# Kernel optimization log

Hardware: AMD Instinct MI355X
Metric: run time of the kernel (lower is better)

Reference implementation:

```python
import jax, jax.numpy as jnp
import numpy as np

S, B, D = 2048, 32, 1024
H = 16
DIM = D // H  # 64 per-head dim
EPS = 1e-5


def setup_inputs() -> dict:
    key = jax.random.key(0)
    k1, k2, k3 = jax.random.split(key, 3)
    src = jax.random.normal(k1, (S, B, D), dtype=jnp.float32)
    # per-head bracket Linear(2*dim -> dim), stacked over heads
    bound = 1.0 / np.sqrt(2 * DIM)
    W = jax.random.uniform(k2, (H, 2 * DIM, DIM), minval=-bound, maxval=bound, dtype=jnp.float32)
    b = jax.random.uniform(k3, (H, DIM), minval=-bound, maxval=bound, dtype=jnp.float32)
    # shared LayerNorm(d_model) params (default init: gamma=1, beta=0)
    gamma = jnp.ones((D,), dtype=jnp.float32)
    beta = jnp.zeros((D,), dtype=jnp.float32)
    return {"src": src, "W": W, "b": b, "gamma": gamma, "beta": beta}


def reference(src, W, b, gamma, beta):
    def layer_norm(x):
        mu = jnp.mean(x, axis=-1, keepdims=True)
        var = jnp.mean(jnp.square(x - mu), axis=-1, keepdims=True)
        return (x - mu) * jax.lax.rsqrt(var + EPS) * gamma + beta

    def step(c, x):
        # c, x: [B, D]; mode='base': y_h = GELU(Linear_h([c_h; x_h])), new context = x
        ch = c.reshape(B, H, DIM)
        xh = x.reshape(B, H, DIM)
        cat = jnp.concatenate([ch, xh], axis=-1)              # [B, H, 2*DIM]
        y = jax.nn.gelu(jnp.einsum('bhk,hkd->bhd', cat, W) + b, approximate=False)
        c_new = layer_norm(x)                                  # LN(context)=LN(x)
        y_out = layer_norm(y.reshape(B, D))
        return c_new, y_out

    c0 = jnp.zeros((B, D), dtype=src.dtype)
    _, ys = jax.lax.scan(step, c0, src)
    return ys  # [S, B, D]
```

## Files before the change

### kernel.cpp

```cpp
#include <hip/hip_runtime.h>

#define SS 2048
#define BB 32
#define DD 1024
#define HH 16

typedef unsigned short u16;
typedef unsigned int u32;
using f32x4 = __attribute__((ext_vector_type(4))) float;
using bf16x8 = __attribute__((ext_vector_type(8))) short;

__device__ __forceinline__ u16 f2bf(float x) {
  union { float f; u32 u; } c; c.f = x;
  u32 r = c.u + 0x7fffu + ((c.u >> 16) & 1u);
  return (u16)(r >> 16);
}
__device__ __forceinline__ float bf2f(u32 h) {
  union { u32 u; float f; } c; c.u = h << 16; return c.f;
}
__device__ __forceinline__ int swzb(int row, int col) {
  return ((row << 11) + (col << 1)) ^ ((row & 7) << 4);
}
__device__ __forceinline__ void st_lds8(u16* base, int row, int col, const u16* v) {
  uint4 pk;
  pk.x = (u32)v[0] | ((u32)v[1] << 16);
  pk.y = (u32)v[2] | ((u32)v[3] << 16);
  pk.z = (u32)v[4] | ((u32)v[5] << 16);
  pk.w = (u32)v[6] | ((u32)v[7] << 16);
  *reinterpret_cast<uint4*>(reinterpret_cast<char*>(base) + swzb(row, col)) = pk;
}
__device__ __forceinline__ uint4 ld_lds8(const u16* base, int row, int col) {
  return *reinterpret_cast<const uint4*>(reinterpret_cast<const char*>(base) + swzb(row, col));
}
__device__ __forceinline__ bf16x8 ld_afrag(const u16* base, int row, int col) {
  return *reinterpret_cast<const bf16x8*>(reinterpret_cast<const char*>(base) + swzb(row, col));
}
__device__ __forceinline__ void st_lds1(u16* base, int row, int col, u16 v) {
  *reinterpret_cast<u16*>(reinterpret_cast<char*>(base) + swzb(row, col)) = v;
}

__global__ void prep_w(const float* __restrict__ W, u16* __restrict__ Wf) {
  const int o = blockIdx.x * 256 + threadIdx.x;
  const int l = o & 63;
  const int tile = o >> 6;
  const int nt = tile & 3, ks = (tile >> 2) & 3, h = tile >> 4;
  const int d = nt * 16 + (l & 15);
  const int kb = ks * 32 + 8 * (l >> 4);
  u16 v[8];
#pragma unroll
  for (int j = 0; j < 8; ++j) v[j] = f2bf(W[(h * 128 + kb + j) * 64 + d]);
  uint4 pk;
  pk.x = (u32)v[0] | ((u32)v[1] << 16);
  pk.y = (u32)v[2] | ((u32)v[3] << 16);
  pk.z = (u32)v[4] | ((u32)v[5] << 16);
  pk.w = (u32)v[6] | ((u32)v[7] << 16);
  reinterpret_cast<uint4*>(Wf)[o] = pk;
}

__global__ __launch_bounds__(1024) void lienet_main(
    const float* __restrict__ src, const u16* __restrict__ Wf,
    const float* __restrict__ bias, const float* __restrict__ gamma,
    const float* __restrict__ beta, float* __restrict__ out) {
  __shared__ __align__(16) u16 cbuf[BB * DD];
  __shared__ __align__(16) u16 xbuf[BB * DD];

  const int bid = blockIdx.x;
  const int t = (bid & 7) * 256 + (bid >> 3);

  const int tid = threadIdx.x;
  const int wave = tid >> 6;
  const int lane = tid & 63;
  const int colbase = lane * 16;

#pragma unroll
  for (int rr = 0; rr < 2; ++rr) {
    const int row = wave * 2 + rr;
    {
      const float4* p = reinterpret_cast<const float4*>(src + ((size_t)t * BB + row) * DD + colbase);
      u16 v[16];
#pragma unroll
      for (int q = 0; q < 4; ++q) {
        float4 f = p[q];
        v[q * 4 + 0] = f2bf(f.x); v[q * 4 + 1] = f2bf(f.y);
        v[q * 4 + 2] = f2bf(f.z); v[q * 4 + 3] = f2bf(f.w);
      }
      st_lds8(xbuf, row, colbase, v);
      st_lds8(xbuf, row, colbase + 8, v + 8);
    }
    if (t == 0) {
      u16 v[16];
#pragma unroll
      for (int j = 0; j < 16; ++j) v[j] = 0;
      st_lds8(cbuf, row, colbase, v);
      st_lds8(cbuf, row, colbase + 8, v + 8);
    } else {
      const float4* p = reinterpret_cast<const float4*>(src + ((size_t)(t - 1) * BB + row) * DD + colbase);
      float f[16];
      float s1 = 0.f, s2 = 0.f;
#pragma unroll
      for (int q = 0; q < 4; ++q) {
        float4 fv = p[q];
        f[q * 4 + 0] = fv.x; f[q * 4 + 1] = fv.y;
        f[q * 4 + 2] = fv.z; f[q * 4 + 3] = fv.w;
      }
#pragma unroll
      for (int j = 0; j < 16; ++j) { s1 += f[j]; s2 += f[j] * f[j]; }
#pragma unroll
      for (int off = 32; off; off >>= 1) { s1 += __shfl_xor(s1, off); s2 += __shfl_xor(s2, off); }
      const float mu = s1 * (1.f / 1024.f);
      const float rs = rsqrtf(s2 * (1.f / 1024.f) - mu * mu + 1e-5f);
      const float4* gp = reinterpret_cast<const float4*>(gamma + colbase);
      const float4* bp = reinterpret_cast<const float4*>(beta + colbase);
      u16 v[16];
#pragma unroll
      for (int q = 0; q < 4; ++q) {
        float4 gv = gp[q], bv = bp[q];
        v[q * 4 + 0] = f2bf((f[q * 4 + 0] - mu) * rs * gv.x + bv.x);
        v[q * 4 + 1] = f2bf((f[q * 4 + 1] - mu) * rs * gv.y + bv.y);
        v[q * 4 + 2] = f2bf((f[q * 4 + 2] - mu) * rs * gv.z + bv.z);
        v[q * 4 + 3] = f2bf((f[q * 4 + 3] - mu) * rs * gv.w + bv.w);
      }
      st_lds8(cbuf, row, colbase, v);
      st_lds8(cbuf, row, colbase + 8, v + 8);
    }
  }
  __syncthreads();

  const int h = wave;
  f32x4 acc[2][4];
#pragma unroll
  for (int mt = 0; mt < 2; ++mt)
#pragma unroll
    for (int nt = 0; nt < 4; ++nt) acc[mt][nt] = (f32x4){0.f, 0.f, 0.f, 0.f};

  const int arow = lane & 15;
  const int kb = 8 * (lane >> 4);
#pragma unroll
  for (int ks = 0; ks < 4; ++ks) {
    const u16* sb = (ks < 2) ? cbuf : xbuf;
    const int col = h * 64 + (ks & 1) * 32 + kb;
    bf16x8 a0 = ld_afrag(sb, arow, col);
    bf16x8 a1 = ld_afrag(sb, arow + 16, col);
    const uint4* wp = reinterpret_cast<const uint4*>(Wf) + ((h * 4 + ks) * 4) * 64 + lane;
#pragma unroll
    for (int nt = 0; nt < 4; ++nt) {
      uint4 wv = wp[nt * 64];
      bf16x8 bfr = *reinterpret_cast<bf16x8*>(&wv);
      acc[0][nt] = __builtin_amdgcn_mfma_f32_16x16x32_bf16(a0, bfr, acc[0][nt], 0, 0, 0);
      acc[1][nt] = __builtin_amdgcn_mfma_f32_16x16x32_bf16(a1, bfr, acc[1][nt], 0, 0, 0);
    }
  }

#pragma unroll
  for (int nt = 0; nt < 4; ++nt) {
    const int dcol = h * 64 + nt * 16 + (lane & 15);
    const float bv = bias[dcol];
#pragma unroll
    for (int mt = 0; mt < 2; ++mt) {
#pragma unroll
      for (int r = 0; r < 4; ++r) {
        const int row = mt * 16 + (lane >> 4) * 4 + r;
        const float v = acc[mt][nt][r] + bv;
        const float gel = 0.5f * v * (1.0f + erff(v * 0.70710678118654752f));
        st_lds1(cbuf, row, dcol, f2bf(gel));
      }
    }
  }
  __syncthreads();

#pragma unroll
  for (int rr = 0; rr < 2; ++rr) {
    const int row = wave * 2 + rr;
    uint4 g0 = ld_lds8(cbuf, row, colbase);
    uint4 g1 = ld_lds8(cbuf, row, colbase + 8);
    float vals[16];
    vals[0] = bf2f(g0.x & 0xffffu); vals[1] = bf2f(g0.x >> 16);
    vals[2] = bf2f(g0.y & 0xffffu); vals[3] = bf2f(g0.y >> 16);
    vals[4] = bf2f(g0.z & 0xffffu); vals[5] = bf2f(g0.z >> 16);
    vals[6] = bf2f(g0.w & 0xffffu); vals[7] = bf2f(g0.w >> 16);
    vals[8] = bf2f(g1.x & 0xffffu); vals[9] = bf2f(g1.x >> 16);
    vals[10] = bf2f(g1.y & 0xffffu); vals[11] = bf2f(g1.y >> 16);
    vals[12] = bf2f(g1.z & 0xffffu); vals[13] = bf2f(g1.z >> 16);
    vals[14] = bf2f(g1.w & 0xffffu); vals[15] = bf2f(g1.w >> 16);
    float s1 = 0.f, s2 = 0.f;
#pragma unroll
    for (int j = 0; j < 16; ++j) { s1 += vals[j]; s2 += vals[j] * vals[j]; }
#pragma unroll
    for (int off = 32; off; off >>= 1) { s1 += __shfl_xor(s1, off); s2 += __shfl_xor(s2, off); }
    const float mu = s1 * (1.f / 1024.f);
    const float rs = rsqrtf(s2 * (1.f / 1024.f) - mu * mu + 1e-5f);
    const float4* gp = reinterpret_cast<const float4*>(gamma + colbase);
    const float4* bp = reinterpret_cast<const float4*>(beta + colbase);
    float* op = out + ((size_t)t * BB + row) * DD + colbase;
#pragma unroll
    for (int q = 0; q < 4; ++q) {
      float4 gv = gp[q], bv = bp[q];
      float4 o;
      o.x = (vals[q * 4 + 0] - mu) * rs * gv.x + bv.x;
      o.y = (vals[q * 4 + 1] - mu) * rs * gv.y + bv.y;
      o.z = (vals[q * 4 + 2] - mu) * rs * gv.z + bv.z;
      o.w = (vals[q * 4 + 3] - mu) * rs * gv.w + bv.w;
      reinterpret_cast<float4*>(op)[q] = o;
    }
  }
}

extern "C" void kernel_launch(void* const* d_in, const int* in_sizes, int n_in,
                              void* d_out, int out_size, void* d_ws, size_t ws_size,
                              hipStream_t stream) {
  const float* src = (const float*)d_in[0];
  const float* W = (const float*)d_in[1];
  const float* bias = (const float*)d_in[2];
  const float* gamma = (const float*)d_in[3];
  const float* beta = (const float*)d_in[4];
  float* out = (float*)d_out;
  u16* Wf = (u16*)d_ws;

  prep_w<<<64, 256, 0, stream>>>(W, Wf);
  lienet_main<<<SS, 1024, 0, stream>>>(src, Wf, bias, gamma, beta, out);
}
```

Before: 258.5 us.

## Split each timestep into 8-row blocks and fuse output LayerNorm in registers

New measurement: 228.4 us. -11.6%, faster.

```diff
diff --git a/kernel.cpp b/kernel.cpp
--- a/kernel.cpp
+++ b/kernel.cpp
@@ -4,6 +4,7 @@
 #define BB 32
 #define DD 1024
 #define HH 16
+#define RB 8
 
 typedef unsigned short u16;
 typedef unsigned int u32;
@@ -15,28 +16,30 @@
   u32 r = c.u + 0x7fffu + ((c.u >> 16) & 1u);
   return (u16)(r >> 16);
 }
-__device__ __forceinline__ float bf2f(u32 h) {
-  union { u32 u; float f; } c; c.u = h << 16; return c.f;
-}
 __device__ __forceinline__ int swzb(int row, int col) {
   return ((row << 11) + (col << 1)) ^ ((row & 7) << 4);
 }
-__device__ __forceinline__ void st_lds8(u16* base, int row, int col, const u16* v) {
+__device__ __forceinline__ void st_lds8(u16* base, int row, int col,
+                                        float4 a, float4 b) {
   uint4 pk;
-  pk.x = (u32)v[0] | ((u32)v[1] << 16);
-  pk.y = (u32)v[2] | ((u32)v[3] << 16);
-  pk.z = (u32)v[4] | ((u32)v[5] << 16);
-  pk.w = (u32)v[6] | ((u32)v[7] << 16);
+  pk.x = (u32)f2bf(a.x) | ((u32)f2bf(a.y) << 16);
+  pk.y = (u32)f2bf(a.z) | ((u32)f2bf(a.w) << 16);
+  pk.z = (u32)f2bf(b.x) | ((u32)f2bf(b.y) << 16);
+  pk.w = (u32)f2bf(b.z) | ((u32)f2bf(b.w) << 16);
   *reinterpret_cast<uint4*>(reinterpret_cast<char*>(base) + swzb(row, col)) = pk;
 }
-__device__ __forceinline__ uint4 ld_lds8(const u16* base, int row, int col) {
-  return *reinterpret_cast<const uint4*>(reinterpret_cast<const char*>(base) + swzb(row, col));
+__device__ __forceinline__ void st_lds8z(u16* base, int row, int col) {
+  uint4 pk; pk.x = pk.y = pk.z = pk.w = 0u;
+  *reinterpret_cast<uint4*>(reinterpret_cast<char*>(base) + swzb(row, col)) = pk;
 }
 __device__ __forceinline__ bf16x8 ld_afrag(const u16* base, int row, int col) {
   return *reinterpret_cast<const bf16x8*>(reinterpret_cast<const char*>(base) + swzb(row, col));
 }
-__device__ __forceinline__ void st_lds1(u16* base, int row, int col, u16 v) {
-  *reinterpret_cast<u16*>(reinterpret_cast<char*>(base) + swzb(row, col)) = v;
+__device__ __forceinline__ float gelu_f(float v) {
+  const float u2 = 1.5957691216057308f * v * __builtin_fmaf(0.044715f, v * v, 1.0f);
+  const float e = __expf(u2);
+  const float th = 1.0f - 2.0f * __builtin_amdgcn_rcpf(e + 1.0f);
+  return 0.5f * v * (1.0f + th);
 }
 
 __global__ void prep_w(const float* __restrict__ W, u16* __restrict__ Wf) {
@@ -57,150 +60,177 @@
   reinterpret_cast<uint4*>(Wf)[o] = pk;
 }
 
-__global__ __launch_bounds__(1024) void lienet_main(
+__global__ __launch_bounds__(256, 4) void lienet_main(
     const float* __restrict__ src, const u16* __restrict__ Wf,
     const float* __restrict__ bias, const float* __restrict__ gamma,
     const float* __restrict__ beta, float* __restrict__ out) {
-  __shared__ __align__(16) u16 cbuf[BB * DD];
-  __shared__ __align__(16) u16 xbuf[BB * DD];
+  __shared__ __align__(16) u16 cbuf[RB * DD];
+  __shared__ __align__(16) u16 xbuf[RB * DD];
+  __shared__ float part[4][RB][2];
 
   const int bid = blockIdx.x;
-  const int t = (bid & 7) * 256 + (bid >> 3);
+  const int lin = (bid & 7) * 1024 + (bid >> 3);
+  const int t = lin >> 2;
+  const int row0 = (lin & 3) * RB;
 
   const int tid = threadIdx.x;
   const int wave = tid >> 6;
   const int lane = tid & 63;
-  const int colbase = lane * 16;
+  const int c0 = lane * 8;
 
 #pragma unroll
   for (int rr = 0; rr < 2; ++rr) {
     const int row = wave * 2 + rr;
+    const int grow = row0 + row;
     {
-      const float4* p = reinterpret_cast<const float4*>(src + ((size_t)t * BB + row) * DD + colbase);
-      u16 v[16];
-#pragma unroll
-      for (int q = 0; q < 4; ++q) {
-        float4 f = p[q];
-        v[q * 4 + 0] = f2bf(f.x); v[q * 4 + 1] = f2bf(f.y);
-        v[q * 4 + 2] = f2bf(f.z); v[q * 4 + 3] = f2bf(f.w);
-      }
-      st_lds8(xbuf, row, colbase, v);
-      st_lds8(xbuf, row, colbase + 8, v + 8);
+      const float* rp = src + ((size_t)t * BB + grow) * DD;
+      float4 f0 = *reinterpret_cast<const float4*>(rp + c0);
+      float4 f1 = *reinterpret_cast<const float4*>(rp + c0 + 4);
+      float4 f2 = *reinterpret_cast<const float4*>(rp + 512 + c0);
+      float4 f3 = *reinterpret_cast<const float4*>(rp + 512 + c0 + 4);
+      st_lds8(xbuf, row, c0, f0, f1);
+      st_lds8(xbuf, row, 512 + c0, f2, f3);
     }
     if (t == 0) {
-      u16 v[16];
-#pragma unroll
-      for (int j = 0; j < 16; ++j) v[j] = 0;
-      st_lds8(cbuf, row, colbase, v);
-      st_lds8(cbuf, row, colbase + 8, v + 8);
+      st_lds8z(cbuf, row, c0);
+      st_lds8z(cbuf, row, 512 + c0);
     } else {
-      const float4* p = reinterpret_cast<const float4*>(src + ((size_t)(t - 1) * BB + row) * DD + colbase);
+      const float* rp = src + ((size_t)(t - 1) * BB + grow) * DD;
       float f[16];
+      *reinterpret_cast<float4*>(f + 0) = *reinterpret_cast<const float4*>(rp + c0);
+      *reinterpret_cast<float4*>(f + 4) = *reinterpret_cast<const float4*>(rp + c0 + 4);
+      *reinterpret_cast<float4*>(f + 8) = *reinterpret_cast<const float4*>(rp + 512 + c0);
+      *reinterpret_cast<float4*>(f + 12) = *reinterpret_cast<const float4*>(rp + 512 + c0 + 4);
       float s1 = 0.f, s2 = 0.f;
-#pragma unroll
-      for (int q = 0; q < 4; ++q) {
-        float4 fv = p[q];
-        f[q * 4 + 0] = fv.x; f[q * 4 + 1] = fv.y;
-        f[q * 4 + 2] = fv.z; f[q * 4 + 3] = fv.w;
-      }
 #pragma unroll
       for (int j = 0; j < 16; ++j) { s1 += f[j]; s2 += f[j] * f[j]; }
 #pragma unroll
       for (int off = 32; off; off >>= 1) { s1 += __shfl_xor(s1, off); s2 += __shfl_xor(s2, off); }
       const float mu = s1 * (1.f / 1024.f);
       const float rs = rsqrtf(s2 * (1.f / 1024.f) - mu * mu + 1e-5f);
-      const float4* gp = reinterpret_cast<const float4*>(gamma + colbase);
-      const float4* bp = reinterpret_cast<const float4*>(beta + colbase);
-      u16 v[16];
-#pragma unroll
-      for (int q = 0; q < 4; ++q) {
-        float4 gv = gp[q], bv = bp[q];
-        v[q * 4 + 0] = f2bf((f[q * 4 + 0] - mu) * rs * gv.x + bv.x);
-        v[q * 4 + 1] = f2bf((f[q * 4 + 1] - mu) * rs * gv.y + bv.y);
-        v[q * 4 + 2] = f2bf((f[q * 4 + 2] - mu) * rs * gv.z + bv.z);
-        v[q * 4 + 3] = f2bf((f[q * 4 + 3] - mu) * rs * gv.w + bv.w);
-      }
-      st_lds8(cbuf, row, colbase, v);
-      st_lds8(cbuf, row, colbase + 8, v + 8);
+      float4 g0 = *reinterpret_cast<const float4*>(gamma + c0);
+      float4 g1 = *reinterpret_cast<const float4*>(gamma + c0 + 4);
+      float4 g2 = *reinterpret_cast<const float4*>(gamma + 512 + c0);
+      float4 g3 = *reinterpret_cast<const float4*>(gamma + 512 + c0 + 4);
+      float4 b0 = *reinterpret_cast<const float4*>(beta + c0);
+      float4 b1 = *reinterpret_cast<const float4*>(beta + c0 + 4);
+      float4 b2 = *reinterpret_cast<const float4*>(beta + 512 + c0);
+      float4 b3 = *reinterpret_cast<const float4*>(beta + 512 + c0 + 4);
+      float4 o0, o1, o2, o3;
+      o0.x = (f[0] - mu) * rs * g0.x + b0.x;  o0.y = (f[1] - mu) * rs * g0.y + b0.y;
+      o0.z = (f[2] - mu) * rs * g0.z + b0.z;  o0.w = (f[3] - mu) * rs * g0.w + b0.w;
+      o1.x = (f[4] - mu) * rs * g1.x + b1.x;  o1.y = (f[5] - mu) * rs * g1.y + b1.y;
+      o1.z = (f[6] - mu) * rs * g1.z + b1.z;  o1.w = (f[7] - mu) * rs * g1.w + b1.w;
+      o2.x = (f[8] - mu) * rs * g2.x + b2.x;  o2.y = (f[9] - mu) * rs * g2.y + b2.y;
+      o2.z = (f[10] - mu) * rs * g2.z + b2.z; o2.w = (f[11] - mu) * rs * g2.w + b2.w;
+      o3.x = (f[12] - mu) * rs * g3.x + b3.x; o3.y = (f[13] - mu) * rs * g3.y + b3.y;
+      o3.z = (f[14] - mu) * rs * g3.z + b3.z; o3.w = (f[15] - mu) * rs * g3.w + b3.w;
+      st_lds8(cbuf, row, c0, o0, o1);
+      st_lds8(cbuf, row, 512 + c0, o2, o3);
     }
   }
   __syncthreads();
 
-  const int h = wave;
-  f32x4 acc[2][4];
-#pragma unroll
-  for (int mt = 0; mt < 2; ++mt)
-#pragma unroll
-    for (int nt = 0; nt < 4; ++nt) acc[mt][nt] = (f32x4){0.f, 0.f, 0.f, 0.f};
-
-  const int arow = lane & 15;
+  f32x4 acc[4][4];
+#pragma unroll
+  for (int hh = 0; hh < 4; ++hh)
+#pragma unroll
+    for (int nt = 0; nt < 4; ++nt) acc[hh][nt] = (f32x4){0.f, 0.f, 0.f, 0.f};
+
+  const int arow = lane & 7;
   const int kb = 8 * (lane >> 4);
 #pragma unroll
   for (int ks = 0; ks < 4; ++ks) {
     const u16* sb = (ks < 2) ? cbuf : xbuf;
-    const int col = h * 64 + (ks & 1) * 32 + kb;
-    bf16x8 a0 = ld_afrag(sb, arow, col);
-    bf16x8 a1 = ld_afrag(sb, arow + 16, col);
-    const uint4* wp = reinterpret_cast<const uint4*>(Wf) + ((h * 4 + ks) * 4) * 64 + lane;
+#pragma unroll
+    for (int hh = 0; hh < 4; ++hh) {
+      const int h = wave * 4 + hh;
+      bf16x8 a = ld_afrag(sb, arow, h * 64 + (ks & 1) * 32 + kb);
+      const uint4* wp = reinterpret_cast<const uint4*>(Wf) + ((h * 4 + ks) * 4) * 64 + lane;
+#pragma unroll
+      for (int nt = 0; nt < 4; ++nt) {
+        uint4 wv = wp[nt * 64];
+        bf16x8 bfr = *reinterpret_cast<bf16x8*>(&wv);
+        acc[hh][nt] = __builtin_amdgcn_mfma_f32_16x16x32_bf16(a, bfr, acc[hh][nt], 0, 0, 0);
+      }
+    }
+  }
+
+  const int hilo = lane >> 5;
+  const int row4 = 4 * ((lane >> 4) & 1);
+  const int cl = lane & 15;
+  float gv[2][4][4];
+#pragma unroll
+  for (int hp = 0; hp < 2; ++hp) {
+    const int h_eff = wave * 4 + hp + 2 * hilo;
 #pragma unroll
     for (int nt = 0; nt < 4; ++nt) {
-      uint4 wv = wp[nt * 64];
-      bf16x8 bfr = *reinterpret_cast<bf16x8*>(&wv);
-      acc[0][nt] = __builtin_amdgcn_mfma_f32_16x16x32_bf16(a0, bfr, acc[0][nt], 0, 0, 0);
-      acc[1][nt] = __builtin_amdgcn_mfma_f32_16x16x32_bf16(a1, bfr, acc[1][nt], 0, 0, 0);
-    }
-  }
-
-#pragma unroll
-  for (int nt = 0; nt < 4; ++nt) {
-    const int dcol = h * 64 + nt * 16 + (lane & 15);
-    const float bv = bias[dcol];
-#pragma unroll
-    for (int mt = 0; mt < 2; ++mt) {
+      const float bv = bias[h_eff * 64 + nt * 16 + cl];
 #pragma unroll
       for (int r = 0; r < 4; ++r) {
-        const int row = mt * 16 + (lane >> 4) * 4 + r;
-        const float v = acc[mt][nt][r] + bv;
-        const float gel = 0.5f * v * (1.0f + erff(v * 0.70710678118654752f));
-        st_lds1(cbuf, row, dcol, f2bf(gel));
-      }
+        const float v = (hilo ? acc[hp + 2][nt][r] : acc[hp][nt][r]) + bv;
+        gv[hp][nt][r] = gelu_f(v);
+      }
+    }
+  }
+  float s1[4], s2[4];
+#pragma unroll
+  for (int r = 0; r < 4; ++r) {
+    float a = 0.f, b = 0.f;
+#pragma unroll
+    for (int hp = 0; hp < 2; ++hp)
+#pragma unroll
+      for (int nt = 0; nt < 4; ++nt) {
+        const float g = gv[hp][nt][r];
+        a += g; b += g * g;
+      }
+    a += __shfl_xor(a, 1); b += __shfl_xor(b, 1);
+    a += __shfl_xor(a, 2); b += __shfl_xor(b, 2);
+    a += __shfl_xor(a, 4); b += __shfl_xor(b, 4);
+    a += __shfl_xor(a, 8); b += __shfl_xor(b, 8);
+    a += __shfl_xor(a, 32); b += __shfl_xor(b, 32);
+    s1[r] = a; s2[r] = b;
+  }
+  if (lane == 0 || lane == 16) {
+#pragma unroll
+    for (int r = 0; r < 4; ++r) {
+      part[wave][row4 + r][0] = s1[r];
+      part[wave][row4 + r][1] = s2[r];
+    }
+  }
+  float gm[2][4], bt[2][4];
+#pragma unroll
+  for (int hp = 0; hp < 2; ++hp) {
+    const int h_eff = wave * 4 + hp + 2 * hilo;
+#pragma unroll
+    for (int nt = 0; nt < 4; ++nt) {
+      const int dcol = h_eff * 64 + nt * 16 + cl;
+      gm[hp][nt] = gamma[dcol];
+      bt[hp][nt] = beta[dcol];
     }
   }
   __syncthreads();
 
-#pragma unroll
-  for (int rr = 0; rr < 2; ++rr) {
-    const int row = wave * 2 + rr;
-    uint4 g0 = ld_lds8(cbuf, row, colbase);
-    uint4 g1 = ld_lds8(cbuf, row, colbase + 8);
-    float vals[16];
-    vals[0] = bf2f(g0.x & 0xffffu); vals[1] = bf2f(g0.x >> 16);
-    vals[2] = bf2f(g0.y & 0xffffu); vals[3] = bf2f(g0.y >> 16);
-    vals[4] = bf2f(g0.z & 0xffffu); vals[5] = bf2f(g0.z >> 16);
-    vals[6] = bf2f(g0.w & 0xffffu); vals[7] = bf2f(g0.w >> 16);
-    vals[8] = bf2f(g1.x & 0xffffu); vals[9] = bf2f(g1.x >> 16);
-    vals[10] = bf2f(g1.y & 0xffffu); vals[11] = bf2f(g1.y >> 16);
-    vals[12] = bf2f(g1.z & 0xffffu); vals[13] = bf2f(g1.z >> 16);
-    vals[14] = bf2f(g1.w & 0xffffu); vals[15] = bf2f(g1.w >> 16);
-    float s1 = 0.f, s2 = 0.f;
-#pragma unroll
-    for (int j = 0; j < 16; ++j) { s1 += vals[j]; s2 += vals[j] * vals[j]; }
-#pragma unroll
-    for (int off = 32; off; off >>= 1) { s1 += __shfl_xor(s1, off); s2 += __shfl_xor(s2, off); }
-    const float mu = s1 * (1.f / 1024.f);
-    const float rs = rsqrtf(s2 * (1.f / 1024.f) - mu * mu + 1e-5f);
-    const float4* gp = reinterpret_cast<const float4*>(gamma + colbase);
-    const float4* bp = reinterpret_cast<const float4*>(beta + colbase);
-    float* op = out + ((size_t)t * BB + row) * DD + colbase;
-#pragma unroll
-    for (int q = 0; q < 4; ++q) {
-      float4 gv = gp[q], bv = bp[q];
-      float4 o;
-      o.x = (vals[q * 4 + 0] - mu) * rs * gv.x + bv.x;
-      o.y = (vals[q * 4 + 1] - mu) * rs * gv.y + bv.y;
-      o.z = (vals[q * 4 + 2] - mu) * rs * gv.z + bv.z;
-      o.w = (vals[q * 4 + 3] - mu) * rs * gv.w + bv.w;
-      reinterpret_cast<float4*>(op)[q] = o;
+  float mu[4], rs[4];
+#pragma unroll
+  for (int r = 0; r < 4; ++r) {
+    const int row = row4 + r;
+    const float a = part[0][row][0] + part[1][row][0] + part[2][row][0] + part[3][row][0];
+    const float b = part[0][row][1] + part[1][row][1] + part[2][row][1] + part[3][row][1];
+    mu[r] = a * (1.f / 1024.f);
+    rs[r] = rsqrtf(b * (1.f / 1024.f) - mu[r] * mu[r] + 1e-5f);
+  }
+#pragma unroll
+  for (int hp = 0; hp < 2; ++hp) {
+    const int h_eff = wave * 4 + hp + 2 * hilo;
+#pragma unroll
+    for (int nt = 0; nt < 4; ++nt) {
+      const int dcol = h_eff * 64 + nt * 16 + cl;
+#pragma unroll
+      for (int r = 0; r < 4; ++r) {
+        const float o = (gv[hp][nt][r] - mu[r]) * rs[r] * gm[hp][nt] + bt[hp][nt];
+        out[((size_t)t * BB + row0 + row4 + r) * DD + dcol] = o;
+      }
     }
   }
 }
@@ -217,5 +247,5 @@
   u16* Wf = (u16*)d_ws;
 
   prep_w<<<64, 256, 0, stream>>>(W, Wf);
-  lienet_main<<<SS, 1024, 0, stream>>>(src, Wf, bias, gamma, beta, out);
-}
+  lienet_main<<<SS * 4, 256, 0, stream>>>(src, Wf, bias, gamma, beta, out);
+}
```
